# Kernel optimization log

Hardware: AMD Instinct MI355X
Metric: run time of the kernel (lower is better)

Reference implementation:

```python
import jax, jax.numpy as jnp
import numpy as np

B, T, E, H = 8, 1024, 128, 8
S = E // H  # 16, narrow per-head dim


def setup_inputs() -> dict:
    key = jax.random.key(0)
    ks = jax.random.split(key, 7)
    return {
        "x": jax.random.normal(ks[0], (B, T, E), dtype=jnp.float32),
        "masks": jax.random.randint(ks[1], (B, T), 0, 2, dtype=jnp.int32),
        "Wq": jax.random.normal(ks[2], (S, S), dtype=jnp.float32) * 0.05,
        "Wk": jax.random.normal(ks[3], (S, S), dtype=jnp.float32) * 0.05,
        "Wv": jax.random.normal(ks[4], (S, S), dtype=jnp.float32) * 0.05,
        "Wu": jax.random.normal(ks[5], (E, E), dtype=jnp.float32) * 0.05,
        "bu": jnp.zeros((E,), dtype=jnp.float32),
        "temporal_only": 1,
    }


def reference(x, masks, Wq, Wk, Wv, Wu, bu, temporal_only):
    b, t, e = x.shape
    h = H
    s = e // h
    x4 = x.reshape(b, t, h, s)
    # nn.Linear(s, s, bias=False): y = x @ W.T, applied per head
    q = jnp.einsum('bths,ds->bthd', x4, Wq)
    k = jnp.einsum('bths,ds->bthd', x4, Wk)
    v = jnp.einsum('bths,ds->bthd', x4, Wv)
    scale = jnp.float32(e) ** 0.25
    q = q / scale
    k = k / scale
    # (b, h, t, t) attention logits
    dot = jnp.einsum('bqhd,bkhd->bhqk', q, k)
    # temporal_only masking: masks is (b, t), applied on key axis then query axis
    m = masks.astype(bool)
    neg = jnp.float32(-1e9)
    dot = jnp.where(m[:, None, None, :], dot, neg)
    dot = jnp.where(m[:, None, :, None], dot, neg)
    attn = jax.nn.softmax(dot, axis=-1)
    # post-softmax zeroing with the same masks
    attn = jnp.where(m[:, None, None, :], attn, jnp.float32(0.0))
    attn = jnp.where(m[:, None, :, None], attn, jnp.float32(0.0))
    out = jnp.einsum('bhqk,bkhd->bqhd', attn, v).reshape(b, t, h * s)
    return out @ Wu.T + bu
```

## Files before the change

### kernel.cpp

```cpp
#include <hip/hip_runtime.h>

#define NB 8
#define NT 1024
#define NE 128
#define NH 8
#define NS 16

#define WS_Q 0
#define WS_K 1048576
#define WS_V 2097152
#define WS_Y 3145728
#define WS_VIDX 4194304

#define WT_PITCH 132

typedef float v2f __attribute__((ext_vector_type(2)));

static __device__ __forceinline__ v2f vlo(const float4 v) { return v2f{v.x, v.y}; }
static __device__ __forceinline__ v2f vhi(const float4 v) { return v2f{v.z, v.w}; }
static __device__ __forceinline__ v2f pfma(v2f a, v2f b, v2f c) {
  return __builtin_elementwise_fma(a, b, c);
}

static __device__ __forceinline__ void fma4(float4& acc, float s, const float4 v) {
  acc.x = fmaf(s, v.x, acc.x);
  acc.y = fmaf(s, v.y, acc.y);
  acc.z = fmaf(s, v.z, acc.z);
  acc.w = fmaf(s, v.w, acc.w);
}

static __device__ __forceinline__ float dot16(const float4 x0, const float4 x1,
                                              const float4 x2, const float4 x3,
                                              const float4 w0, const float4 w1,
                                              const float4 w2, const float4 w3) {
  float s0 = (x0.x * w0.x + x0.y * w0.y) + (x0.z * w0.z + x0.w * w0.w);
  float s1 = (x1.x * w1.x + x1.y * w1.y) + (x1.z * w1.z + x1.w * w1.w);
  float s2 = (x2.x * w2.x + x2.y * w2.y) + (x2.z * w2.z + x2.w * w2.w);
  float s3 = (x3.x * w3.x + x3.y * w3.y) + (x3.z * w3.z + x3.w * w3.w);
  return (s0 + s1) + (s2 + s3);
}

static __device__ __forceinline__ float dot16p(const float4 q0, const float4 q1,
                                               const float4 q2, const float4 q3,
                                               const float4 k0, const float4 k1,
                                               const float4 k2, const float4 k3) {
  v2f a = vlo(q0) * vlo(k0);
  v2f b = vhi(q0) * vhi(k0);
  a = pfma(vlo(q1), vlo(k1), a);
  b = pfma(vhi(q1), vhi(k1), b);
  a = pfma(vlo(q2), vlo(k2), a);
  b = pfma(vhi(q2), vhi(k2), b);
  a = pfma(vlo(q3), vlo(k3), a);
  b = pfma(vhi(q3), vhi(k3), b);
  v2f c = a + b;
  return c.x + c.y;
}

__global__ __launch_bounds__(256) void qkv_kernel(
    const float* __restrict__ x, const int* __restrict__ masks,
    const float* __restrict__ Wq, const float* __restrict__ Wk,
    const float* __restrict__ Wv, float* __restrict__ Q, float* __restrict__ K,
    float* __restrict__ V, int* __restrict__ vidx, int* __restrict__ vcount) {
  if (blockIdx.x >= 1024) {
    const int b = blockIdx.x - 1024;
    const int lane = threadIdx.x;
    if (lane < 64) {
      int base = 0;
      for (int c = 0; c < NT; c += 64) {
        int t = c + lane;
        int v = masks[b * NT + t] != 0;
        unsigned long long bal = __ballot(v);
        int pos = base + __popcll(bal & ((1ull << lane) - 1ull));
        if (v) vidx[b * NT + pos] = t;
        base += __popcll(bal);
      }
      if (lane == 0) vcount[b] = base;
    }
    return;
  }
  const int tid = threadIdx.x;
  const int h = blockIdx.x & 7;
  const int rg = blockIdx.x >> 3;
  const int b = rg >> 4;
  const int base = rg << 6;
  const int d = tid & 15;
  const int r = base + ((tid >> 4) << 2);
  const float4* wq4 = (const float4*)(Wq + d * 16);
  const float4 wq0 = wq4[0], wq1 = wq4[1], wq2 = wq4[2], wq3 = wq4[3];
  const float4* wk4 = (const float4*)(Wk + d * 16);
  const float4 wk0 = wk4[0], wk1 = wk4[1], wk2 = wk4[2], wk3 = wk4[3];
  const float4* wv4 = (const float4*)(Wv + d * 16);
  const float4 wv0 = wv4[0], wv1 = wv4[1], wv2 = wv4[2], wv3 = wv4[3];
  const float invs = 0.08838834764831845f;
#pragma unroll
  for (int i = 0; i < 4; i++) {
    const int row = r + i;
    const float4* xp = (const float4*)(x + (size_t)row * 128 + h * 16);
    const float4 x0 = xp[0], x1 = xp[1], x2 = xp[2], x3 = xp[3];
    float aq = dot16(x0, x1, x2, x3, wq0, wq1, wq2, wq3);
    float ak = dot16(x0, x1, x2, x3, wk0, wk1, wk2, wk3);
    float av = dot16(x0, x1, x2, x3, wv0, wv1, wv2, wv3);
    const int t = row & 1023;
    size_t o = ((size_t)(b * NH + h) * NT + t) * NS + d;
    Q[o] = aq * invs;
    K[o] = ak;
    V[o] = av;
  }
}

__global__ __launch_bounds__(256) void attn_kernel(
    const float* __restrict__ Q, const float* __restrict__ K,
    const float* __restrict__ V, const int* __restrict__ masks,
    const int* __restrict__ vidx, const int* __restrict__ vcount,
    float* __restrict__ Y) {
  __shared__ __align__(16) float Ks[2048];
  __shared__ __align__(16) float Vs[2048];
  __shared__ __align__(16) float om[2][4][64][20];
  __shared__ float ml[2][4][64][2];
  const int tid = threadIdx.x;
  const int lane = tid & 63;
  const int split = tid >> 6;
  const int bh = blockIdx.x >> 3;
  const int b = bh >> 3, h = bh & 7;
  const int tbase = (blockIdx.x & 7) << 7;
  const int tA = tbase + lane;
  const int nv = vcount[b];
  const float4* qga = (const float4*)(Q + ((size_t)bh * NT + tA) * NS);
  const float4 qa0 = qga[0], qa1 = qga[1], qa2 = qga[2], qa3 = qga[3];
  const float4* qgb = (const float4*)(Q + ((size_t)bh * NT + tA + 64) * NS);
  const float4 qb0 = qgb[0], qb1 = qgb[1], qb2 = qgb[2], qb3 = qgb[3];
  float mA = -1e30f, lA = 0.f, mB = -1e30f, lB = 0.f;
  v2f oa[8], ob[8];
#pragma unroll
  for (int j = 0; j < 8; j++) { oa[j] = v2f{0.f, 0.f}; ob[j] = v2f{0.f, 0.f}; }

  for (int k0 = 0; k0 < nv; k0 += 128) {
    __syncthreads();
    const int quad = tid & 3;
    const int jr = tid >> 2;
#pragma unroll
    for (int p = 0; p < 2; p++) {
      int row = jr + (p << 6);
      int j = k0 + row;
      float4 kv = {0, 0, 0, 0}, vv = {0, 0, 0, 0};
      if (j < nv) {
        int kk = vidx[b * NT + j];
        size_t bse = ((size_t)bh * NT + kk) * NS + (quad << 2);
        kv = *(const float4*)(K + bse);
        vv = *(const float4*)(V + bse);
      }
      *(float4*)(Ks + row * 16 + (quad << 2)) = kv;
      *(float4*)(Vs + row * 16 + (quad << 2)) = vv;
    }
    __syncthreads();
    int jmax = nv - k0;
    if (jmax > 128) jmax = 128;
    for (int g = 0; g < 8; g++) {
      const int rbase = split + (g << 4);
      if (rbase >= jmax) break;
      float sA[4], sB[4];
#pragma unroll
      for (int i = 0; i < 4; i++) {
        const float4* kr = (const float4*)(Ks + (rbase + (i << 2)) * 16);
        float4 k0v = kr[0], k1v = kr[1], k2v = kr[2], k3v = kr[3];
        sA[i] = dot16p(qa0, qa1, qa2, qa3, k0v, k1v, k2v, k3v);
        sB[i] = dot16p(qb0, qb1, qb2, qb3, k0v, k1v, k2v, k3v);
      }
#pragma unroll
      for (int i = 0; i < 4; i++)
        if (rbase + (i << 2) >= jmax) { sA[i] = -1e30f; sB[i] = -1e30f; }
      float mbA = fmaxf(fmaxf(sA[0], sA[1]), fmaxf(sA[2], sA[3]));
      if (mbA > mA) {
        float al = __expf(mA - mbA);
        v2f al2 = {al, al};
        lA *= al;
#pragma unroll
        for (int j = 0; j < 8; j++) oa[j] *= al2;
        mA = mbA;
      }
      float pA[4];
      pA[0] = __expf(sA[0] - mA); pA[1] = __expf(sA[1] - mA);
      pA[2] = __expf(sA[2] - mA); pA[3] = __expf(sA[3] - mA);
      lA += (pA[0] + pA[1]) + (pA[2] + pA[3]);
      float mbB = fmaxf(fmaxf(sB[0], sB[1]), fmaxf(sB[2], sB[3]));
      if (mbB > mB) {
        float al = __expf(mB - mbB);
        v2f al2 = {al, al};
        lB *= al;
#pragma unroll
        for (int j = 0; j < 8; j++) ob[j] *= al2;
        mB = mbB;
      }
      float pB[4];
      pB[0] = __expf(sB[0] - mB); pB[1] = __expf(sB[1] - mB);
      pB[2] = __expf(sB[2] - mB); pB[3] = __expf(sB[3] - mB);
      lB += (pB[0] + pB[1]) + (pB[2] + pB[3]);
#pragma unroll
      for (int i = 0; i < 4; i++) {
        const float4* vr = (const float4*)(Vs + (rbase + (i << 2)) * 16);
        float4 v0 = vr[0], v1 = vr[1], v2 = vr[2], v3 = vr[3];
        const v2f pa2 = {pA[i], pA[i]};
        const v2f pb2 = {pB[i], pB[i]};
        oa[0] = pfma(pa2, vlo(v0), oa[0]); oa[1] = pfma(pa2, vhi(v0), oa[1]);
        oa[2] = pfma(pa2, vlo(v1), oa[2]); oa[3] = pfma(pa2, vhi(v1), oa[3]);
        oa[4] = pfma(pa2, vlo(v2), oa[4]); oa[5] = pfma(pa2, vhi(v2), oa[5]);
        oa[6] = pfma(pa2, vlo(v3), oa[6]); oa[7] = pfma(pa2, vhi(v3), oa[7]);
        ob[0] = pfma(pb2, vlo(v0), ob[0]); ob[1] = pfma(pb2, vhi(v0), ob[1]);
        ob[2] = pfma(pb2, vlo(v1), ob[2]); ob[3] = pfma(pb2, vhi(v1), ob[3]);
        ob[4] = pfma(pb2, vlo(v2), ob[4]); ob[5] = pfma(pb2, vhi(v2), ob[5]);
        ob[6] = pfma(pb2, vlo(v3), ob[6]); ob[7] = pfma(pb2, vhi(v3), ob[7]);
      }
    }
  }
  ml[0][split][lane][0] = mA; ml[0][split][lane][1] = lA;
  ml[1][split][lane][0] = mB; ml[1][split][lane][1] = lB;
  {
    float* pa = &om[0][split][lane][0];
#pragma unroll
    for (int j = 0; j < 8; j++) *(v2f*)(pa + j * 2) = oa[j];
    float* pb = &om[1][split][lane][0];
#pragma unroll
    for (int j = 0; j < 8; j++) *(v2f*)(pb + j * 2) = ob[j];
  }
  __syncthreads();
  if (split < 2) {
    const int qg = split;
    const int tq = tbase + (qg << 6) + lane;
    float m0 = ml[qg][0][lane][0], l0 = ml[qg][0][lane][1];
    float m1 = ml[qg][1][lane][0], l1 = ml[qg][1][lane][1];
    float m2 = ml[qg][2][lane][0], l2 = ml[qg][2][lane][1];
    float m3 = ml[qg][3][lane][0], l3 = ml[qg][3][lane][1];
    float M = fmaxf(fmaxf(m0, m1), fmaxf(m2, m3));
    float f0 = __expf(m0 - M), f1 = __expf(m1 - M), f2 = __expf(m2 - M),
          f3 = __expf(m3 - M);
    float L = f0 * l0 + f1 * l1 + f2 * l2 + f3 * l3;
    float4 y0 = {0, 0, 0, 0}, y1 = {0, 0, 0, 0}, y2 = {0, 0, 0, 0},
           y3 = {0, 0, 0, 0};
    float fs[4] = {f0, f1, f2, f3};
#pragma unroll
    for (int s = 0; s < 4; s++) {
      const float* p = &om[qg][s][lane][0];
      fma4(y0, fs[s], *(const float4*)(p + 0));
      fma4(y1, fs[s], *(const float4*)(p + 4));
      fma4(y2, fs[s], *(const float4*)(p + 8));
      fma4(y3, fs[s], *(const float4*)(p + 12));
    }
    const int qm = masks[b * NT + tq];
    const float inv = (qm != 0 && L > 0.f) ? (1.0f / L) : 0.f;
    y0.x *= inv; y0.y *= inv; y0.z *= inv; y0.w *= inv;
    y1.x *= inv; y1.y *= inv; y1.z *= inv; y1.w *= inv;
    y2.x *= inv; y2.y *= inv; y2.z *= inv; y2.w *= inv;
    y3.x *= inv; y3.y *= inv; y3.z *= inv; y3.w *= inv;
    float4* yo = (float4*)(Y + ((size_t)b * NT + tq) * NE + h * NS);
    yo[0] = y0; yo[1] = y1; yo[2] = y2; yo[3] = y3;
  }
}

__global__ __launch_bounds__(256) void proj_kernel(
    const float* __restrict__ Y, const float* __restrict__ Wu,
    const float* __restrict__ bu, float* __restrict__ out) {
  __shared__ __align__(16) float Wt[64 * WT_PITCH];
  __shared__ __align__(16) float Yt[16 * 128];
  const int tid = threadIdx.x;
  const int r0 = blockIdx.x * 16;
  const float4* yg = (const float4*)(Y + (size_t)r0 * 128);
  float4* yt4 = (float4*)Yt;
  yt4[tid] = yg[tid];
  yt4[tid + 256] = yg[tid + 256];
  const int c0 = (tid & 31) << 2;
  const int rg = (tid >> 5) & 3;
  const int eh = tid >> 7;
  float4 acc0 = {0, 0, 0, 0}, acc1 = {0, 0, 0, 0}, acc2 = {0, 0, 0, 0},
         acc3 = {0, 0, 0, 0};
  for (int e0 = 0; e0 < 128; e0 += 64) {
    __syncthreads();
#pragma unroll
    for (int p = 0; p < 8; p++) {
      int idx = tid + p * 256;
      int c = idx >> 4;
      int es = (idx & 15) << 2;
      float4 w = *(const float4*)(Wu + c * 128 + e0 + es);
      Wt[(es + 0) * WT_PITCH + c] = w.x;
      Wt[(es + 1) * WT_PITCH + c] = w.y;
      Wt[(es + 2) * WT_PITCH + c] = w.z;
      Wt[(es + 3) * WT_PITCH + c] = w.w;
    }
    __syncthreads();
    const int eb = eh << 5;
    const float* y0 = Yt + (rg * 4 + 0) * 128 + e0 + eb;
    const float* y1 = Yt + (rg * 4 + 1) * 128 + e0 + eb;
    const float* y2 = Yt + (rg * 4 + 2) * 128 + e0 + eb;
    const float* y3 = Yt + (rg * 4 + 3) * 128 + e0 + eb;
#pragma unroll 4
    for (int e = 0; e < 32; e += 4) {
      const float* wb = Wt + (eb + e) * WT_PITCH + c0;
      float4 w0 = *(const float4*)(wb + 0 * WT_PITCH);
      float4 w1 = *(const float4*)(wb + 1 * WT_PITCH);
      float4 w2 = *(const float4*)(wb + 2 * WT_PITCH);
      float4 w3 = *(const float4*)(wb + 3 * WT_PITCH);
      float4 ya = *(const float4*)(y0 + e);
      float4 yb = *(const float4*)(y1 + e);
      float4 yc = *(const float4*)(y2 + e);
      float4 yd = *(const float4*)(y3 + e);
      fma4(acc0, ya.x, w0); fma4(acc0, ya.y, w1); fma4(acc0, ya.z, w2); fma4(acc0, ya.w, w3);
      fma4(acc1, yb.x, w0); fma4(acc1, yb.y, w1); fma4(acc1, yb.z, w2); fma4(acc1, yb.w, w3);
      fma4(acc2, yc.x, w0); fma4(acc2, yc.y, w1); fma4(acc2, yc.z, w2); fma4(acc2, yc.w, w3);
      fma4(acc3, yd.x, w0); fma4(acc3, yd.y, w1); fma4(acc3, yd.z, w2); fma4(acc3, yd.w, w3);
    }
  }
  __syncthreads();
  if (eh == 1) {
    float* p = Wt + (tid & 127) * 20;
    *(float4*)(p + 0) = acc0; *(float4*)(p + 4) = acc1;
    *(float4*)(p + 8) = acc2; *(float4*)(p + 12) = acc3;
  }
  __syncthreads();
  if (eh == 0) {
    const float* p = Wt + tid * 20;
    float4 b4 = *(const float4*)(bu + c0);
    float4 q0 = *(const float4*)(p + 0);
    float4 q1 = *(const float4*)(p + 4);
    float4 q2 = *(const float4*)(p + 8);
    float4 q3 = *(const float4*)(p + 12);
    acc0.x += q0.x + b4.x; acc0.y += q0.y + b4.y; acc0.z += q0.z + b4.z; acc0.w += q0.w + b4.w;
    acc1.x += q1.x + b4.x; acc1.y += q1.y + b4.y; acc1.z += q1.z + b4.z; acc1.w += q1.w + b4.w;
    acc2.x += q2.x + b4.x; acc2.y += q2.y + b4.y; acc2.z += q2.z + b4.z; acc2.w += q2.w + b4.w;
    acc3.x += q3.x + b4.x; acc3.y += q3.y + b4.y; acc3.z += q3.z + b4.z; acc3.w += q3.w + b4.w;
    *(float4*)(out + (size_t)(r0 + rg * 4 + 0) * 128 + c0) = acc0;
    *(float4*)(out + (size_t)(r0 + rg * 4 + 1) * 128 + c0) = acc1;
    *(float4*)(out + (size_t)(r0 + rg * 4 + 2) * 128 + c0) = acc2;
    *(float4*)(out + (size_t)(r0 + rg * 4 + 3) * 128 + c0) = acc3;
  }
}

extern "C" void kernel_launch(void* const* d_in, const int* in_sizes, int n_in,
                              void* d_out, int out_size, void* d_ws,
                              size_t ws_size, hipStream_t stream) {
  const float* x = (const float*)d_in[0];
  const int* masks = (const int*)d_in[1];
  const float* Wq = (const float*)d_in[2];
  const float* Wk = (const float*)d_in[3];
  const float* Wv = (const float*)d_in[4];
  const float* Wu = (const float*)d_in[5];
  const float* bu = (const float*)d_in[6];
  float* out = (float*)d_out;

  float* ws = (float*)d_ws;
  float* Q = ws + WS_Q;
  float* K = ws + WS_K;
  float* V = ws + WS_V;
  float* Y = ws + WS_Y;
  int* vidx = (int*)(ws + WS_VIDX);
  int* vcount = vidx + NB * NT;

  qkv_kernel<<<1024 + NB, 256, 0, stream>>>(x, masks, Wq, Wk, Wv, Q, K, V,
                                            vidx, vcount);
  attn_kernel<<<NB * NH * (NT / 128), 256, 0, stream>>>(Q, K, V, masks, vidx,
                                                        vcount, Y);
  proj_kernel<<<NB * NT / 16, 256, 0, stream>>>(Y, Wu, bu, out);
}
```

Measured before the change: 136.9 us.

## Restructure attention to 4 queries per thread with wave-uniform direct K/V loads

Reworks the attention kernel to 512-thread blocks covering 256 queries. Each thread now holds 4 query rows, and the key set is split across 8 waves. K/V rows are read straight from global memory through wave-uniform indices taken with readlane, replacing the shared-memory staging and its barriers. The 8 partial softmax states are merged through LDS in four phases, and the QKV projection and fma4 helper switch to packed FMA. This raises per-key reuse of the K/V loads and removes the per-tile syncs, at the cost of higher register pressure (64 q floats plus 64 accumulators) and scalar-addressed global loads that may expose more latency.

```diff
diff --git a/kernel.cpp b/kernel.cpp
--- a/kernel.cpp
+++ b/kernel.cpp
@@ -23,21 +23,9 @@
 }
 
 static __device__ __forceinline__ void fma4(float4& acc, float s, const float4 v) {
-  acc.x = fmaf(s, v.x, acc.x);
-  acc.y = fmaf(s, v.y, acc.y);
-  acc.z = fmaf(s, v.z, acc.z);
-  acc.w = fmaf(s, v.w, acc.w);
-}
-
-static __device__ __forceinline__ float dot16(const float4 x0, const float4 x1,
-                                              const float4 x2, const float4 x3,
-                                              const float4 w0, const float4 w1,
-                                              const float4 w2, const float4 w3) {
-  float s0 = (x0.x * w0.x + x0.y * w0.y) + (x0.z * w0.z + x0.w * w0.w);
-  float s1 = (x1.x * w1.x + x1.y * w1.y) + (x1.z * w1.z + x1.w * w1.w);
-  float s2 = (x2.x * w2.x + x2.y * w2.y) + (x2.z * w2.z + x2.w * w2.w);
-  float s3 = (x3.x * w3.x + x3.y * w3.y) + (x3.z * w3.z + x3.w * w3.w);
-  return (s0 + s1) + (s2 + s3);
+  v2f lo = pfma(v2f{s, s}, vlo(v), vlo(acc));
+  v2f hi = pfma(v2f{s, s}, vhi(v), vhi(acc));
+  acc.x = lo.x; acc.y = lo.y; acc.z = hi.x; acc.w = hi.y;
 }
 
 static __device__ __forceinline__ float dot16p(const float4 q0, const float4 q1,
@@ -97,9 +85,9 @@
     const int row = r + i;
     const float4* xp = (const float4*)(x + (size_t)row * 128 + h * 16);
     const float4 x0 = xp[0], x1 = xp[1], x2 = xp[2], x3 = xp[3];
-    float aq = dot16(x0, x1, x2, x3, wq0, wq1, wq2, wq3);
-    float ak = dot16(x0, x1, x2, x3, wk0, wk1, wk2, wk3);
-    float av = dot16(x0, x1, x2, x3, wv0, wv1, wv2, wv3);
+    float aq = dot16p(x0, x1, x2, x3, wq0, wq1, wq2, wq3);
+    float ak = dot16p(x0, x1, x2, x3, wk0, wk1, wk2, wk3);
+    float av = dot16p(x0, x1, x2, x3, wv0, wv1, wv2, wv3);
     const int t = row & 1023;
     size_t o = ((size_t)(b * NH + h) * NT + t) * NS + d;
     Q[o] = aq * invs;
@@ -108,151 +96,139 @@
   }
 }
 
-__global__ __launch_bounds__(256) void attn_kernel(
+__global__ __launch_bounds__(512) void attn_kernel(
     const float* __restrict__ Q, const float* __restrict__ K,
     const float* __restrict__ V, const int* __restrict__ masks,
     const int* __restrict__ vidx, const int* __restrict__ vcount,
     float* __restrict__ Y) {
-  __shared__ __align__(16) float Ks[2048];
-  __shared__ __align__(16) float Vs[2048];
-  __shared__ __align__(16) float om[2][4][64][20];
-  __shared__ float ml[2][4][64][2];
+  __shared__ __align__(16) float om[8 * 64 * 20];
   const int tid = threadIdx.x;
   const int lane = tid & 63;
-  const int split = tid >> 6;
-  const int bh = blockIdx.x >> 3;
+  const int s = tid >> 6;
+  const int bh = blockIdx.x >> 2;
   const int b = bh >> 3, h = bh & 7;
-  const int tbase = (blockIdx.x & 7) << 7;
-  const int tA = tbase + lane;
-  const int nv = vcount[b];
-  const float4* qga = (const float4*)(Q + ((size_t)bh * NT + tA) * NS);
-  const float4 qa0 = qga[0], qa1 = qga[1], qa2 = qga[2], qa3 = qga[3];
-  const float4* qgb = (const float4*)(Q + ((size_t)bh * NT + tA + 64) * NS);
-  const float4 qb0 = qgb[0], qb1 = qgb[1], qb2 = qgb[2], qb3 = qgb[3];
-  float mA = -1e30f, lA = 0.f, mB = -1e30f, lB = 0.f;
-  v2f oa[8], ob[8];
-#pragma unroll
-  for (int j = 0; j < 8; j++) { oa[j] = v2f{0.f, 0.f}; ob[j] = v2f{0.f, 0.f}; }
-
-  for (int k0 = 0; k0 < nv; k0 += 128) {
+  const int tbase = (blockIdx.x & 3) << 8;
+  const int nv = __builtin_amdgcn_readfirstlane(vcount[b]);
+
+  float4 q[4][4];
+#pragma unroll
+  for (int qq = 0; qq < 4; qq++) {
+    const float4* qg =
+        (const float4*)(Q + ((size_t)bh * NT + tbase + (qq << 6) + lane) * NS);
+    q[qq][0] = qg[0]; q[qq][1] = qg[1]; q[qq][2] = qg[2]; q[qq][3] = qg[3];
+  }
+  v2f o[4][8];
+  float m[4], l[4];
+#pragma unroll
+  for (int qq = 0; qq < 4; qq++) {
+    m[qq] = -1e30f; l[qq] = 0.f;
+#pragma unroll
+    for (int k = 0; k < 8; k++) o[qq][k] = v2f{0.f, 0.f};
+  }
+
+  const int p0 = s + (lane << 3);
+  const int idx0 = (p0 < nv) ? vidx[b * NT + p0] : 0;
+  const int idx1 = (p0 + 512 < nv) ? vidx[b * NT + p0 + 512] : 0;
+  const float* Kb = K + (size_t)bh * NT * NS;
+  const float* Vb = V + (size_t)bh * NT * NS;
+
+#pragma unroll 1
+  for (int r0 = 0; s + (r0 << 3) < nv; r0 += 4) {
+    float sc[4][4];
+    int kks[4];
+#pragma unroll
+    for (int i = 0; i < 4; i++) {
+      const int r = r0 + i;
+      const int kk = (r < 64) ? __builtin_amdgcn_readlane(idx0, r)
+                              : __builtin_amdgcn_readlane(idx1, r - 64);
+      kks[i] = kk;
+      const float4* kp = (const float4*)(Kb + (size_t)kk * NS);
+      const float4 k0 = kp[0], k1 = kp[1], k2 = kp[2], k3 = kp[3];
+#pragma unroll
+      for (int qq = 0; qq < 4; qq++)
+        sc[qq][i] = dot16p(q[qq][0], q[qq][1], q[qq][2], q[qq][3], k0, k1, k2, k3);
+    }
+#pragma unroll
+    for (int i = 0; i < 4; i++)
+      if (s + ((r0 + i) << 3) >= nv) {
+        sc[0][i] = -1e30f; sc[1][i] = -1e30f;
+        sc[2][i] = -1e30f; sc[3][i] = -1e30f;
+      }
+    float p[4][4];
+#pragma unroll
+    for (int qq = 0; qq < 4; qq++) {
+      float mb = fmaxf(fmaxf(sc[qq][0], sc[qq][1]), fmaxf(sc[qq][2], sc[qq][3]));
+      if (mb > m[qq]) {
+        float al = __expf(m[qq] - mb);
+        v2f al2 = {al, al};
+        l[qq] *= al;
+#pragma unroll
+        for (int k = 0; k < 8; k++) o[qq][k] *= al2;
+        m[qq] = mb;
+      }
+      p[qq][0] = __expf(sc[qq][0] - m[qq]);
+      p[qq][1] = __expf(sc[qq][1] - m[qq]);
+      p[qq][2] = __expf(sc[qq][2] - m[qq]);
+      p[qq][3] = __expf(sc[qq][3] - m[qq]);
+      l[qq] += (p[qq][0] + p[qq][1]) + (p[qq][2] + p[qq][3]);
+    }
+#pragma unroll
+    for (int i = 0; i < 4; i++) {
+      const float4* vp = (const float4*)(Vb + (size_t)kks[i] * NS);
+      const float4 v0 = vp[0], v1 = vp[1], v2 = vp[2], v3 = vp[3];
+#pragma unroll
+      for (int qq = 0; qq < 4; qq++) {
+        const v2f pq = {p[qq][i], p[qq][i]};
+        o[qq][0] = pfma(pq, vlo(v0), o[qq][0]);
+        o[qq][1] = pfma(pq, vhi(v0), o[qq][1]);
+        o[qq][2] = pfma(pq, vlo(v1), o[qq][2]);
+        o[qq][3] = pfma(pq, vhi(v1), o[qq][3]);
+        o[qq][4] = pfma(pq, vlo(v2), o[qq][4]);
+        o[qq][5] = pfma(pq, vhi(v2), o[qq][5]);
+        o[qq][6] = pfma(pq, vlo(v3), o[qq][6]);
+        o[qq][7] = pfma(pq, vhi(v3), o[qq][7]);
+      }
+    }
+  }
+
+#pragma unroll
+  for (int ph = 0; ph < 4; ph++) {
     __syncthreads();
-    const int quad = tid & 3;
-    const int jr = tid >> 2;
-#pragma unroll
-    for (int p = 0; p < 2; p++) {
-      int row = jr + (p << 6);
-      int j = k0 + row;
-      float4 kv = {0, 0, 0, 0}, vv = {0, 0, 0, 0};
-      if (j < nv) {
-        int kk = vidx[b * NT + j];
-        size_t bse = ((size_t)bh * NT + kk) * NS + (quad << 2);
-        kv = *(const float4*)(K + bse);
-        vv = *(const float4*)(V + bse);
-      }
-      *(float4*)(Ks + row * 16 + (quad << 2)) = kv;
-      *(float4*)(Vs + row * 16 + (quad << 2)) = vv;
+    {
+      float* pa = om + (s * 64 + lane) * 20;
+#pragma unroll
+      for (int k = 0; k < 8; k++) *(v2f*)(pa + k * 2) = o[ph][k];
+      pa[16] = m[ph];
+      pa[17] = l[ph];
     }
     __syncthreads();
-    int jmax = nv - k0;
-    if (jmax > 128) jmax = 128;
-    for (int g = 0; g < 8; g++) {
-      const int rbase = split + (g << 4);
-      if (rbase >= jmax) break;
-      float sA[4], sB[4];
-#pragma unroll
-      for (int i = 0; i < 4; i++) {
-        const float4* kr = (const float4*)(Ks + (rbase + (i << 2)) * 16);
-        float4 k0v = kr[0], k1v = kr[1], k2v = kr[2], k3v = kr[3];
-        sA[i] = dot16p(qa0, qa1, qa2, qa3, k0v, k1v, k2v, k3v);
-        sB[i] = dot16p(qb0, qb1, qb2, qb3, k0v, k1v, k2v, k3v);
-      }
-#pragma unroll
-      for (int i = 0; i < 4; i++)
-        if (rbase + (i << 2) >= jmax) { sA[i] = -1e30f; sB[i] = -1e30f; }
-      float mbA = fmaxf(fmaxf(sA[0], sA[1]), fmaxf(sA[2], sA[3]));
-      if (mbA > mA) {
-        float al = __expf(mA - mbA);
-        v2f al2 = {al, al};
-        lA *= al;
-#pragma unroll
-        for (int j = 0; j < 8; j++) oa[j] *= al2;
-        mA = mbA;
-      }
-      float pA[4];
-      pA[0] = __expf(sA[0] - mA); pA[1] = __expf(sA[1] - mA);
-      pA[2] = __expf(sA[2] - mA); pA[3] = __expf(sA[3] - mA);
-      lA += (pA[0] + pA[1]) + (pA[2] + pA[3]);
-      float mbB = fmaxf(fmaxf(sB[0], sB[1]), fmaxf(sB[2], sB[3]));
-      if (mbB > mB) {
-        float al = __expf(mB - mbB);
-        v2f al2 = {al, al};
-        lB *= al;
-#pragma unroll
-        for (int j = 0; j < 8; j++) ob[j] *= al2;
-        mB = mbB;
-      }
-      float pB[4];
-      pB[0] = __expf(sB[0] - mB); pB[1] = __expf(sB[1] - mB);
-      pB[2] = __expf(sB[2] - mB); pB[3] = __expf(sB[3] - mB);
-      lB += (pB[0] + pB[1]) + (pB[2] + pB[3]);
-#pragma unroll
-      for (int i = 0; i < 4; i++) {
-        const float4* vr = (const float4*)(Vs + (rbase + (i << 2)) * 16);
-        float4 v0 = vr[0], v1 = vr[1], v2 = vr[2], v3 = vr[3];
-        const v2f pa2 = {pA[i], pA[i]};
-        const v2f pb2 = {pB[i], pB[i]};
-        oa[0] = pfma(pa2, vlo(v0), oa[0]); oa[1] = pfma(pa2, vhi(v0), oa[1]);
-        oa[2] = pfma(pa2, vlo(v1), oa[2]); oa[3] = pfma(pa2, vhi(v1), oa[3]);
-        oa[4] = pfma(pa2, vlo(v2), oa[4]); oa[5] = pfma(pa2, vhi(v2), oa[5]);
-        oa[6] = pfma(pa2, vlo(v3), oa[6]); oa[7] = pfma(pa2, vhi(v3), oa[7]);
-        ob[0] = pfma(pb2, vlo(v0), ob[0]); ob[1] = pfma(pb2, vhi(v0), ob[1]);
-        ob[2] = pfma(pb2, vlo(v1), ob[2]); ob[3] = pfma(pb2, vhi(v1), ob[3]);
-        ob[4] = pfma(pb2, vlo(v2), ob[4]); ob[5] = pfma(pb2, vhi(v2), ob[5]);
-        ob[6] = pfma(pb2, vlo(v3), ob[6]); ob[7] = pfma(pb2, vhi(v3), ob[7]);
-      }
-    }
-  }
-  ml[0][split][lane][0] = mA; ml[0][split][lane][1] = lA;
-  ml[1][split][lane][0] = mB; ml[1][split][lane][1] = lB;
-  {
-    float* pa = &om[0][split][lane][0];
-#pragma unroll
-    for (int j = 0; j < 8; j++) *(v2f*)(pa + j * 2) = oa[j];
-    float* pb = &om[1][split][lane][0];
-#pragma unroll
-    for (int j = 0; j < 8; j++) *(v2f*)(pb + j * 2) = ob[j];
-  }
-  __syncthreads();
-  if (split < 2) {
-    const int qg = split;
-    const int tq = tbase + (qg << 6) + lane;
-    float m0 = ml[qg][0][lane][0], l0 = ml[qg][0][lane][1];
-    float m1 = ml[qg][1][lane][0], l1 = ml[qg][1][lane][1];
-    float m2 = ml[qg][2][lane][0], l2 = ml[qg][2][lane][1];
-    float m3 = ml[qg][3][lane][0], l3 = ml[qg][3][lane][1];
-    float M = fmaxf(fmaxf(m0, m1), fmaxf(m2, m3));
-    float f0 = __expf(m0 - M), f1 = __expf(m1 - M), f2 = __expf(m2 - M),
-          f3 = __expf(m3 - M);
-    float L = f0 * l0 + f1 * l1 + f2 * l2 + f3 * l3;
-    float4 y0 = {0, 0, 0, 0}, y1 = {0, 0, 0, 0}, y2 = {0, 0, 0, 0},
-           y3 = {0, 0, 0, 0};
-    float fs[4] = {f0, f1, f2, f3};
-#pragma unroll
-    for (int s = 0; s < 4; s++) {
-      const float* p = &om[qg][s][lane][0];
-      fma4(y0, fs[s], *(const float4*)(p + 0));
-      fma4(y1, fs[s], *(const float4*)(p + 4));
-      fma4(y2, fs[s], *(const float4*)(p + 8));
-      fma4(y3, fs[s], *(const float4*)(p + 12));
-    }
-    const int qm = masks[b * NT + tq];
-    const float inv = (qm != 0 && L > 0.f) ? (1.0f / L) : 0.f;
-    y0.x *= inv; y0.y *= inv; y0.z *= inv; y0.w *= inv;
-    y1.x *= inv; y1.y *= inv; y1.z *= inv; y1.w *= inv;
-    y2.x *= inv; y2.y *= inv; y2.z *= inv; y2.w *= inv;
-    y3.x *= inv; y3.y *= inv; y3.z *= inv; y3.w *= inv;
-    float4* yo = (float4*)(Y + ((size_t)b * NT + tq) * NE + h * NS);
-    yo[0] = y0; yo[1] = y1; yo[2] = y2; yo[3] = y3;
+    {
+      const int q8 = tid >> 3;
+      const int sub = tid & 7;
+      float ms[8], ls[8];
+#pragma unroll
+      for (int ss = 0; ss < 8; ss++) {
+        const float* pp = om + (ss * 64 + q8) * 20;
+        ms[ss] = pp[16];
+        ls[ss] = pp[17];
+      }
+      float M = fmaxf(fmaxf(fmaxf(ms[0], ms[1]), fmaxf(ms[2], ms[3])),
+                      fmaxf(fmaxf(ms[4], ms[5]), fmaxf(ms[6], ms[7])));
+      float L = 0.f;
+      v2f y = {0.f, 0.f};
+#pragma unroll
+      for (int ss = 0; ss < 8; ss++) {
+        float f = __expf(ms[ss] - M);
+        L = fmaf(f, ls[ss], L);
+        v2f ov = *(const v2f*)(om + (ss * 64 + q8) * 20 + sub * 2);
+        y = pfma(v2f{f, f}, ov, y);
+      }
+      const int tq = tbase + (ph << 6) + q8;
+      const int qm = masks[b * NT + tq];
+      const float inv = (qm != 0 && L > 0.f) ? (1.0f / L) : 0.f;
+      y *= v2f{inv, inv};
+      *(v2f*)(Y + ((size_t)b * NT + tq) * NE + h * NS + sub * 2) = y;
+    }
   }
 }
 
@@ -355,7 +331,7 @@
 
   qkv_kernel<<<1024 + NB, 256, 0, stream>>>(x, masks, Wq, Wk, Wv, Q, K, V,
                                             vidx, vcount);
-  attn_kernel<<<NB * NH * (NT / 128), 256, 0, stream>>>(Q, K, V, masks, vidx,
+  attn_kernel<<<NB * NH * (NT / 256), 512, 0, stream>>>(Q, K, V, masks, vidx,
                                                         vcount, Y);
   proj_kernel<<<NB * NT / 16, 256, 0, stream>>>(Y, Wu, bu, out);
 }
```

After: 146.6 us. 1.07x slower.
